# Kernel optimization log

Hardware: AMD Instinct MI355X
Metric: run time of the kernel (lower is better)

The kernel has to match this reference:

```python
import jax, jax.numpy as jnp
import numpy as np

B, C, N = 8, 128, 32768


def setup_inputs() -> dict:
    key = jax.random.key(0)
    ks = jax.random.split(key, 16)
    def g(k, shape, scale=0.05):
        return jax.random.normal(k, shape, dtype=jnp.float32) * scale
    return {
        "x": jax.random.normal(ks[0], (B, C, N), dtype=jnp.float32),
        "y": jax.random.normal(ks[1], (B, C, N), dtype=jnp.float32),
        "q_w": g(ks[2], (C, C)), "q_b": g(ks[3], (C,)),
        "k_w": g(ks[4], (C, C)), "k_b": g(ks[5], (C,)),
        "v1_w": g(ks[6], (C, C)), "v1_b": g(ks[7], (C,)),
        "v2_w": g(ks[8], (C, C)), "v2_b": g(ks[9], (C,)),
        "t1_w": g(ks[10], (2 * C, 2 * C)), "t1_b": g(ks[11], (2 * C,)),
        "t2_w": g(ks[12], (C, 2 * C)), "t2_b": g(ks[13], (C,)),
    }


def reference(x, y, q_w, q_b, k_w, k_b, v1_w, v1_b, v2_w, v2_b,
              t1_w, t1_b, t2_w, t2_b):
    # num_heads = 1, head_dim = C. Conv1d with kernel 1 == pointwise matmul.
    c = x.shape[1]
    pconv = lambda w, b, z: jnp.einsum('oc,bcn->bon', w, z) + b[None, :, None]
    x_q = pconv(q_w, q_b, y)    # [B,C,N]
    x_k = pconv(k_w, k_b, x)    # [B,C,N]
    x_v = pconv(v1_w, v1_b, x)  # [B,C,N]
    y_v = pconv(v2_w, v2_b, y)  # [B,C,N]
    x_con = jnp.concatenate([x_q, x_k], axis=1)                 # [B,2C,N]
    v_con = jnp.concatenate([y_v.transpose(0, 2, 1),
                             x_v.transpose(0, 2, 1)], axis=2)   # [B,N,2C]
    scale = jnp.sqrt(jnp.float32(2 * c))
    energy = jnp.einsum('bcn,bdn->bcd', x_con, x_con) / scale   # [B,2C,2C]
    e = jax.nn.relu(energy @ t1_w.T + t1_b)                     # [B,2C,2C]
    e = jax.nn.relu(e @ t2_w.T + t2_b)                          # [B,2C,C]
    attn = jax.nn.softmax(e, axis=-1)                           # [B,2C,C]
    x_r = jnp.einsum('bnd,bdc->bnc', v_con, attn)               # [B,N,C]
    return x_r.transpose(0, 2, 1)                               # [B,C,N]
```

## Files before the change

### kernel.cpp

```cpp
#include <hip/hip_runtime.h>

constexpr int CH   = 128;
constexpr int TWOC = 256;
constexpr int NPTS = 32768;
constexpr int NB   = 8;
constexpr int KC   = 2048;

constexpr int KC3    = 1024;
constexpr int KSTAGE = 128;
constexpr int NST    = KC3 / KSTAGE;
constexpr int NCHUNK = NPTS / KC3;

typedef _Float16 half8 __attribute__((ext_vector_type(8)));
typedef float floatx4 __attribute__((ext_vector_type(4)));

constexpr size_t OFF_G  = 0;
constexpr size_t OFF_S  = 524288;
constexpr size_t OFF_P  = 526336;
constexpr size_t OFF_H  = 528384;
constexpr size_t OFF_E  = 1052672;
constexpr size_t OFF_E1 = 1576960;
constexpr size_t OFF_E2 = 2101248;
constexpr size_t OFF_AT = 2363392;
constexpr size_t OFF_C0 = 2625536;
constexpr size_t OFF_MH = 2626560;
constexpr size_t OFF_ZH = 2757632;
constexpr size_t OFF_GP = OFF_ZH + 33554432;
constexpr size_t GP_LEN = (size_t)3 * NB * NCHUNK * 128 * 128;
constexpr size_t WS_NEED_NEW = (OFF_ZH + 33554432) * sizeof(float);
constexpr size_t WS_NEED_V3  = (OFF_GP + GP_LEN) * sizeof(float);


__global__ __launch_bounds__(256) void convert_kernel(
    const float* __restrict__ x, const float* __restrict__ y,
    _Float16* __restrict__ Zh, float* __restrict__ S)
{
  const int seg = blockIdx.x;
  const int r   = blockIdx.y;
  const int b   = blockIdx.z;
  const float* src = ((r < CH) ? (y + ((size_t)b*CH + r)*NPTS)
                               : (x + ((size_t)b*CH + (r-CH))*NPTS)) + (size_t)seg*4096;
  _Float16* dst = Zh + ((size_t)b*TWOC + r)*NPTS + (size_t)seg*4096;
  const int tid = threadIdx.x;

  float s = 0.f;
  #pragma unroll
  for (int it = 0; it < 4; it++) {
    const int idx = it*1024 + tid*4;
    const float4 v = *(const float4*)(src + idx);
    union { uint2 u; _Float16 h[4]; } p;
    p.h[0]=(_Float16)v.x; p.h[1]=(_Float16)v.y; p.h[2]=(_Float16)v.z; p.h[3]=(_Float16)v.w;
    *(uint2*)(dst + idx) = p.u;
    s += v.x + v.y + v.z + v.w;
  }

  for (int off = 32; off > 0; off >>= 1) s += __shfl_down(s, off);
  if ((tid & 63) == 0) atomicAdd(&S[b*TWOC + r], s);
}

__global__ __launch_bounds__(256) void gram_mfma3(
    const _Float16* __restrict__ Zh, float* __restrict__ G, float* __restrict__ GP)
{
  __shared__ __align__(16) _Float16 As[2][128 * KSTAGE];
  __shared__ __align__(16) _Float16 Bs[2][128 * KSTAGE];

  const int hw    = blockIdx.x;
  const int xcd   = hw & 7;
  const int local = hw >> 3;
  const int t     = local % 3;
  const int grp   = local / 3;
  const int gidx  = xcd * 32 + grp;
  const int kc    = gidx & 31;
  const int b     = gidx >> 5;

  const int i0 = (t == 0) ? 0 : CH;
  const int j0 = (t == 2) ? CH : 0;
  const _Float16* Ar = Zh + ((size_t)b*TWOC + i0)*NPTS + (size_t)kc*KC3;
  const _Float16* Br = Zh + ((size_t)b*TWOC + j0)*NPTS + (size_t)kc*KC3;

  const int tid   = threadIdx.x;
  const int lane  = tid & 63;
  const int wave  = tid >> 6;
  const int mbase = (wave & 1) * 64;
  const int nbase = (wave >> 1) * 64;
  const int m0    = lane & 15;
  const int quad  = lane >> 4;

#define STAGE(buf, k0)                                                        \
  {                                                                           \
    _Pragma("unroll")                                                         \
    for (int i = 0; i < 8; i++) {                                             \
      const int s = wave*512 + i*64 + lane;                                   \
      const int r = s >> 4;                                                   \
      const int g = s & 15;                                                   \
      const int gs = g ^ (r & 7);                                             \
      __builtin_amdgcn_global_load_lds(                                       \
        (const __attribute__((address_space(1))) void*)(Ar + (size_t)r*NPTS + (k0) + gs*8), \
        (__attribute__((address_space(3))) void*)&As[buf][(wave*512 + i*64)*8], \
        16, 0, 0);                                                            \
      __builtin_amdgcn_global_load_lds(                                       \
        (const __attribute__((address_space(1))) void*)(Br + (size_t)r*NPTS + (k0) + gs*8), \
        (__attribute__((address_space(3))) void*)&Bs[buf][(wave*512 + i*64)*8], \
        16, 0, 0);                                                            \
    }                                                                         \
  }

  floatx4 acc[4][4];
  #pragma unroll
  for (int i = 0; i < 4; i++)
    #pragma unroll
    for (int j = 0; j < 4; j++) acc[i][j] = (floatx4){0.f,0.f,0.f,0.f};

  STAGE(0, 0);

  int cur = 0;
  for (int st = 0; st < NST; ++st) {
    if (st + 1 < NST) {
      STAGE(cur ^ 1, (st + 1) * KSTAGE);
      asm volatile("s_waitcnt vmcnt(16)" ::: "memory");
    } else {
      asm volatile("s_waitcnt vmcnt(0)" ::: "memory");
    }
    __builtin_amdgcn_s_barrier();

    #pragma unroll
    for (int kk = 0; kk < 4; kk++) {
      half8 af[4], bf[4];
      #pragma unroll
      for (int i = 0; i < 4; i++) {
        const int ra = mbase + i*16 + m0;
        const int ga = (kk*4 + quad) ^ (ra & 7);
        af[i] = *(const half8*)&As[cur][ra*KSTAGE + ga*8];
        const int rb = nbase + i*16 + m0;
        const int gb = (kk*4 + quad) ^ (rb & 7);
        bf[i] = *(const half8*)&Bs[cur][rb*KSTAGE + gb*8];
      }
      #pragma unroll
      for (int i = 0; i < 4; i++)
        #pragma unroll
        for (int j = 0; j < 4; j++)
          acc[i][j] = __builtin_amdgcn_mfma_f32_16x16x32_f16(af[i], bf[j], acc[i][j], 0, 0, 0);
    }

    __builtin_amdgcn_s_barrier();
    cur ^= 1;
  }
#undef STAGE

  if (GP != nullptr) {
    float* gp = GP + (((size_t)(b*3 + t)*NCHUNK + kc) * (128*128));
    #pragma unroll
    for (int i = 0; i < 4; i++)
      #pragma unroll
      for (int j = 0; j < 4; j++)
        #pragma unroll
        for (int rg = 0; rg < 4; rg++) {
          const int row = mbase + i*16 + quad*4 + rg;
          const int col = nbase + j*16 + m0;
          gp[row*128 + col] = acc[i][j][rg];
        }
  } else {
    #pragma unroll
    for (int i = 0; i < 4; i++)
      #pragma unroll
      for (int j = 0; j < 4; j++)
        #pragma unroll
        for (int rg = 0; rg < 4; rg++) {
          const int row = i0 + mbase + i*16 + quad*4 + rg;
          const int col = j0 + nbase + j*16 + m0;
          atomicAdd(&G[((size_t)b*TWOC + row)*TWOC + col], acc[i][j][rg]);
        }
  }
}

__global__ __launch_bounds__(256) void greduce_kernel(
    const float* __restrict__ GP, float* __restrict__ G)
{
  const int t   = blockIdx.y;
  const int b   = blockIdx.z;
  const int idx = blockIdx.x * 256 + threadIdx.x;
  const float* gp = GP + ((size_t)(b*3 + t)*NCHUNK) * (128*128) + idx;
  float s = 0.f;
  #pragma unroll
  for (int k = 0; k < NCHUNK; k++) s += gp[(size_t)k * (128*128)];
  const int i0 = (t == 0) ? 0 : CH;
  const int j0 = (t == 2) ? CH : 0;
  const int row = idx >> 7, col = idx & 127;
  G[((size_t)b*TWOC + i0 + row)*TWOC + j0 + col] = s;
  if (t == 1)
    G[((size_t)b*TWOC + col)*TWOC + CH + row] = s;
}

__global__ __launch_bounds__(256) void att_row_kernel(
    const float* __restrict__ G, const float* __restrict__ S,
    const float* __restrict__ qw, const float* __restrict__ kw,
    const float* __restrict__ qb, const float* __restrict__ kb,
    const float* __restrict__ t1w, const float* __restrict__ t1b,
    const float* __restrict__ t2w, const float* __restrict__ t2b,
    float* __restrict__ ATT)
{
  const int i   = blockIdx.x;
  const int b   = blockIdx.y;
  const int tid = threadIdx.x;

  __shared__ float Hs[TWOC];
  __shared__ float Es[TWOC];
  __shared__ float E1s[TWOC];
  __shared__ float Ss[TWOC];
  __shared__ float red[8];

  Ss[tid] = S[b*TWOC + tid];

  const int jbase = (i < CH) ? 0 : CH;
  const float* wi  = (i < CH) ? (qw + (size_t)i*CH) : (kw + (size_t)(i-CH)*CH);
  const float bci  = (i < CH) ? qb[i] : kb[i-CH];

  float hacc = 0.f;
  const float* gcol = G + ((size_t)b*TWOC + jbase)*TWOC + tid;
  for (int j2 = 0; j2 < CH; j2++) hacc = fmaf(wi[j2], gcol[(size_t)j2*TWOC], hacc);
  Hs[tid] = hacc;
  __syncthreads();

  {
    const int j = tid;
    const float* wj = (j < CH) ? (qw + (size_t)j*CH) : (kw + (size_t)(j-CH)*CH);
    const float bcj = (j < CH) ? qb[j] : kb[j-CH];
    const float* hseg = Hs + ((j < CH) ? 0 : CH);
    const float* ssj  = Ss + ((j < CH) ? 0 : CH);
    const float* ssi  = Ss + ((i < CH) ? 0 : CH);
    const float4* w4  = (const float4*)wj;
    const float4* wi4 = (const float4*)wi;
    float eacc = 0.f, pj = 0.f, pi = 0.f;
    for (int k = 0; k < CH/4; k++) {
      const float4 wv  = w4[k];
      const float4 hv  = *(const float4*)&hseg[k*4];
      const float4 sv  = *(const float4*)&ssj[k*4];
      const float4 wiv = wi4[k];
      const float4 siv = *(const float4*)&ssi[k*4];
      eacc += hv.x*wv.x + hv.y*wv.y + hv.z*wv.z + hv.w*wv.w;
      pj   += sv.x*wv.x + sv.y*wv.y + sv.z*wv.z + sv.w*wv.w;
      pi   += siv.x*wiv.x + siv.y*wiv.y + siv.z*wiv.z + siv.w*wiv.w;
    }
    eacc += pi*bcj + bci*pj + (float)NPTS * bci * bcj;
    Es[j] = eacc * (1.0f/16.0f);
  }
  __syncthreads();

  {
    float a1 = t1b[tid];
    const float4* wr = (const float4*)(t1w + (size_t)tid*TWOC);
    for (int k = 0; k < TWOC/4; k++) {
      const float4 wv = wr[k];
      const float4 ev = *(const float4*)&Es[k*4];
      a1 += ev.x*wv.x + ev.y*wv.y + ev.z*wv.z + ev.w*wv.w;
    }
    E1s[tid] = fmaxf(a1, 0.f);
  }
  __syncthreads();

  float e2 = 0.f;
  if (tid < CH) {
    float a2 = t2b[tid];
    const float4* wr = (const float4*)(t2w + (size_t)tid*TWOC);
    for (int k = 0; k < TWOC/4; k++) {
      const float4 wv = wr[k];
      const float4 ev = *(const float4*)&E1s[k*4];
      a2 += ev.x*wv.x + ev.y*wv.y + ev.z*wv.z + ev.w*wv.w;
    }
    e2 = fmaxf(a2, 0.f);
  }

  const int lane = tid & 63, wv_ = tid >> 6;
  float m = (tid < CH) ? e2 : -1e30f;
  for (int off = 32; off > 0; off >>= 1) m = fmaxf(m, __shfl_xor(m, off));
  if (lane == 0) red[wv_] = m;
  __syncthreads();
  m = fmaxf(red[0], red[1]);

  float ex = (tid < CH) ? expf(e2 - m) : 0.f;
  float sum = ex;
  for (int off = 32; off > 0; off >>= 1) sum += __shfl_xor(sum, off);
  if (lane == 0) red[4 + wv_] = sum;
  __syncthreads();
  sum = red[4] + red[5];

  if (tid < CH)
    ATT[((size_t)b*TWOC + i)*CH + tid] = ex / sum;
}

__global__ __launch_bounds__(256) void out_mfma(
    const _Float16* __restrict__ Zh, const _Float16* __restrict__ Mh,
    const float* __restrict__ C0, float* __restrict__ out)
{
  const int n0 = blockIdx.x * 128;
  const int b  = blockIdx.y;

  __shared__ __align__(16) _Float16 As[128*64];
  __shared__ __align__(16) _Float16 Bs[128*72];

  const int tid   = threadIdx.x;
  const int lane  = tid & 63;
  const int wave  = tid >> 6;
  const int mbase = (wave & 1) * 64;
  const int nbase = (wave >> 1) * 64;
  const int m0    = lane & 15;
  const int quad  = lane >> 4;

  const int srow  = tid >> 1;
  const int gbase = (tid & 1) * 4;
  const int dl    = tid >> 4;
  const int ng    = tid & 15;

  floatx4 acc[4][4];
  #pragma unroll
  for (int i = 0; i < 4; i++)
    #pragma unroll
    for (int j = 0; j < 4; j++) acc[i][j] = (floatx4){0.f,0.f,0.f,0.f};

  for (int d0 = 0; d0 < TWOC; d0 += 64) {
    __syncthreads();
    #pragma unroll
    for (int q = 0; q < 4; q++) {
      const int g  = gbase + q;
      const int gp = g ^ (srow & 7);
      *(uint4*)&As[(size_t)(srow*8 + gp)*8] =
          *(const uint4*)(Mh + ((size_t)b*CH + srow)*TWOC + d0 + g*8);
    }
    #pragma unroll
    for (int ds = 0; ds < 4; ds++) {
      const int d    = dl + ds*16;
      const int gd   = d >> 3;
      const int dlow = d & 7;
      union { uint4 u; _Float16 h[8]; } v;
      v.u = *(const uint4*)(Zh + ((size_t)b*TWOC + d0 + d)*NPTS + n0 + ng*8);
      #pragma unroll
      for (int e = 0; e < 8; e++) {
        const int n  = ng*8 + e;
        const int pg = gd ^ (ng & 7);
        Bs[(size_t)n*72 + pg*8 + dlow] = v.h[e];
      }
    }
    __syncthreads();
    #pragma unroll
    for (int ks = 0; ks < 2; ks++) {
      half8 af[4], bf[4];
      #pragma unroll
      for (int i = 0; i < 4; i++) {
        const int ra = mbase + i*16 + m0;
        const int ga = (ks*4 + quad) ^ (ra & 7);
        af[i] = *(const half8*)&As[(size_t)(ra*8 + ga)*8];
        const int rn  = nbase + i*16 + m0;
        const int g   = ks*4 + quad;
        const int pgr = g ^ ((rn >> 3) & 7);
        bf[i] = *(const half8*)&Bs[(size_t)rn*72 + pgr*8];
      }
      #pragma unroll
      for (int i = 0; i < 4; i++)
        #pragma unroll
        for (int j = 0; j < 4; j++)
          acc[i][j] = __builtin_amdgcn_mfma_f32_16x16x32_f16(af[i], bf[j], acc[i][j], 0, 0, 0);
    }
  }

  #pragma unroll
  for (int i = 0; i < 4; i++) {
    #pragma unroll
    for (int rg = 0; rg < 4; rg++) {
      const int c  = mbase + i*16 + quad*4 + rg;
      const float cv = C0[b*CH + c];
      #pragma unroll
      for (int j = 0; j < 4; j++) {
        const int n = n0 + nbase + j*16 + m0;
        out[((size_t)b*CH + c)*NPTS + n] = acc[i][j][rg] + cv;
      }
    }
  }
}

__global__ void mout_f16_kernel(const float* __restrict__ ATT, const float* __restrict__ v1w,
                                const float* __restrict__ v2w, const float* __restrict__ v1b,
                                const float* __restrict__ v2b, _Float16* __restrict__ Mh,
                                float* __restrict__ C0)
{
  const int c = blockIdx.x, b = blockIdx.y, j = threadIdx.x;
  __shared__ float acol[TWOC];
  acol[j] = ATT[((size_t)b*TWOC + j)*CH + c];
  __syncthreads();
  float acc = 0.f;
  if (j < CH) {
    for (int d = 0; d < CH; d++) acc = fmaf(acol[d], v2w[(size_t)d*CH + j], acc);
  } else {
    const int jj = j - CH;
    for (int d = 0; d < CH; d++) acc = fmaf(acol[CH + d], v1w[(size_t)d*CH + jj], acc);
  }
  Mh[((size_t)b*CH + c)*TWOC + j] = (_Float16)acc;
  if (j == 0) {
    float s = 0.f;
    for (int d = 0; d < CH; d++) s += acol[d]*v2b[d] + acol[CH+d]*v1b[d];
    C0[b*CH + c] = s;
  }
}

__global__ void pmirror_kernel(const float* __restrict__ S, const float* __restrict__ qw,
                               const float* __restrict__ kw, float* __restrict__ P,
                               float* __restrict__ G)
{
  const int b = blockIdx.x;
  const int tid = threadIdx.x;
  float* Gb = G + (size_t)b * TWOC * TWOC;
  for (int idx = tid; idx < CH*CH; idx += 256) {
    const int i2 = idx >> 7, j2 = idx & 127;
    Gb[(size_t)i2*TWOC + CH + j2] = Gb[(size_t)(CH + j2)*TWOC + i2];
  }
}

__global__ __launch_bounds__(256) void gram_kernel(
    const float* __restrict__ x, const float* __restrict__ y,
    float* __restrict__ G, float* __restrict__ S)
{
  const int t  = blockIdx.x;
  const int kc = blockIdx.y;
  const int b  = blockIdx.z;
  const float* Ab = (t == 0) ? y : x;
  const float* Bb = (t == 2) ? x : y;
  const int growA = (t == 0) ? 0 : CH;
  const int gcolB = (t == 2) ? CH : 0;
  const float* Ap = Ab + (size_t)b * CH * NPTS + (size_t)kc * KC;
  const float* Bp = Bb + (size_t)b * CH * NPTS + (size_t)kc * KC;

  __shared__ __align__(16) float As[8][128];
  __shared__ __align__(16) float Bs[8][128];

  const int tid  = threadIdx.x;
  const int ti   = tid >> 4;
  const int tj   = tid & 15;
  const int lrow = tid >> 1;
  const int lk4  = (tid & 1) * 4;

  const float* arow = Ap + (size_t)lrow * NPTS + lk4;
  const float* brow = Bp + (size_t)lrow * NPTS + lk4;

  float acc[8][8];
  #pragma unroll
  for (int i = 0; i < 8; i++)
    #pragma unroll
    for (int j = 0; j < 8; j++) acc[i][j] = 0.f;
  float asum = 0.f;

  for (int k0 = 0; k0 < KC; k0 += 8) {
    const float4 av = *(const float4*)(arow + k0);
    const float4 bv = *(const float4*)(brow + k0);
    __syncthreads();
    As[lk4+0][lrow] = av.x; As[lk4+1][lrow] = av.y;
    As[lk4+2][lrow] = av.z; As[lk4+3][lrow] = av.w;
    Bs[lk4+0][lrow] = bv.x; Bs[lk4+1][lrow] = bv.y;
    Bs[lk4+2][lrow] = bv.z; Bs[lk4+3][lrow] = bv.w;
    asum += av.x + av.y + av.z + av.w;
    __syncthreads();
    #pragma unroll
    for (int kk = 0; kk < 8; kk++) {
      float a[8], bb[8];
      *(float4*)&a[0]  = *(const float4*)&As[kk][ti*8];
      *(float4*)&a[4]  = *(const float4*)&As[kk][ti*8+4];
      *(float4*)&bb[0] = *(const float4*)&Bs[kk][tj*8];
      *(float4*)&bb[4] = *(const float4*)&Bs[kk][tj*8+4];
      #pragma unroll
      for (int ii = 0; ii < 8; ii++)
        #pragma unroll
        for (int jj = 0; jj < 8; jj++)
          acc[ii][jj] = fmaf(a[ii], bb[jj], acc[ii][jj]);
    }
  }

  float* Gp = G + ((size_t)b * TWOC + growA) * TWOC + gcolB;
  #pragma unroll
  for (int ii = 0; ii < 8; ii++)
    #pragma unroll
    for (int jj = 0; jj < 8; jj++)
      atomicAdd(&Gp[(size_t)(ti*8+ii) * TWOC + (tj*8+jj)], acc[ii][jj]);

  if (t == 0)      atomicAdd(&S[b*TWOC + lrow],      asum);
  else if (t == 2) atomicAdd(&S[b*TWOC + CH + lrow], asum);
}

__global__ void mout_f32_kernel(const float* __restrict__ ATT, const float* __restrict__ v1w,
                                const float* __restrict__ v2w, const float* __restrict__ v1b,
                                const float* __restrict__ v2b, float* __restrict__ M,
                                float* __restrict__ C0)
{
  const int c = blockIdx.x, b = blockIdx.y, j = threadIdx.x;
  __shared__ float acol[TWOC];
  acol[j] = ATT[((size_t)b*TWOC + j)*CH + c];
  __syncthreads();
  float acc = 0.f;
  if (j < CH) {
    for (int d = 0; d < CH; d++) acc = fmaf(acol[d], v2w[(size_t)d*CH + j], acc);
  } else {
    const int jj = j - CH;
    for (int d = 0; d < CH; d++) acc = fmaf(acol[CH + d], v1w[(size_t)d*CH + jj], acc);
  }
  M[((size_t)b*CH + c)*TWOC + j] = acc;
  if (j == 0) {
    float s = 0.f;
    for (int d = 0; d < CH; d++) s += acol[d]*v2b[d] + acol[CH+d]*v1b[d];
    C0[b*CH + c] = s;
  }
}

__global__ __launch_bounds__(256) void out_kernel(
    const float* __restrict__ x, const float* __restrict__ y,
    const float* __restrict__ M, const float* __restrict__ C0,
    float* __restrict__ out)
{
  const int b  = blockIdx.y;
  const int n0 = blockIdx.x * 64;
  const int tid = threadIdx.x;
  const int tc = tid & 15;
  const int tn = tid >> 4;

  __shared__ __align__(16) float Ms[64][128];
  __shared__ __align__(16) float Zs[64][64];

  float acc[8][4];
  #pragma unroll
  for (int i = 0; i < 8; i++)
    #pragma unroll
    for (int j = 0; j < 4; j++) acc[i][j] = 0.f;

  const float* Mb = M + (size_t)b * CH * TWOC;

  for (int chunk = 0; chunk < 4; chunk++) {
    const int kbase = chunk * 64;
    const float* Zsrc = ((chunk < 2) ? y : x) + (size_t)b * CH * NPTS
                        + (size_t)((chunk & 1) * 64) * NPTS;
    __syncthreads();
    {
      const int c   = tid >> 1;
      const int kb2 = (tid & 1) * 32;
      const float* mr = Mb + (size_t)c * TWOC + kbase + kb2;
      #pragma unroll
      for (int q = 0; q < 8; q++) {
        const float4 v = *(const float4*)(mr + q*4);
        Ms[kb2 + q*4 + 0][c] = v.x;
        Ms[kb2 + q*4 + 1][c] = v.y;
        Ms[kb2 + q*4 + 2][c] = v.z;
        Ms[kb2 + q*4 + 3][c] = v.w;
      }
      const int kk  = tid >> 2;
      const int nb4 = (tid & 3) * 4;
      const float* zr = Zsrc + (size_t)kk * NPTS + n0 + nb4;
      #pragma unroll
      for (int q = 0; q < 4; q++)
        *(float4*)&Zs[kk][nb4 + q*16] = *(const float4*)(zr + q*16);
    }
    __syncthreads();
    #pragma unroll 8
    for (int kk = 0; kk < 64; kk++) {
      float a[8], zz[4];
      *(float4*)&a[0]  = *(const float4*)&Ms[kk][tc*8];
      *(float4*)&a[4]  = *(const float4*)&Ms[kk][tc*8+4];
      *(float4*)&zz[0] = *(const float4*)&Zs[kk][tn*4];
      #pragma unroll
      for (int ii = 0; ii < 8; ii++)
        #pragma unroll
        for (int jj = 0; jj < 4; jj++)
          acc[ii][jj] = fmaf(a[ii], zz[jj], acc[ii][jj]);
    }
  }

  #pragma unroll
  for (int ii = 0; ii < 8; ii++) {
    const int c = tc*8 + ii;
    const float cv = C0[b*CH + c];
    float4 o;
    o.x = acc[ii][0] + cv; o.y = acc[ii][1] + cv;
    o.z = acc[ii][2] + cv; o.w = acc[ii][3] + cv;
    *(float4*)&out[((size_t)b*CH + c)*NPTS + n0 + tn*4] = o;
  }
}

extern "C" void kernel_launch(void* const* d_in, const int* in_sizes, int n_in,
                              void* d_out, int out_size, void* d_ws, size_t ws_size,
                              hipStream_t stream)
{
  const float* x   = (const float*)d_in[0];
  const float* y   = (const float*)d_in[1];
  const float* qw  = (const float*)d_in[2];
  const float* qb  = (const float*)d_in[3];
  const float* kw  = (const float*)d_in[4];
  const float* kb  = (const float*)d_in[5];
  const float* v1w = (const float*)d_in[6];
  const float* v1b = (const float*)d_in[7];
  const float* v2w = (const float*)d_in[8];
  const float* v2b = (const float*)d_in[9];
  const float* t1w = (const float*)d_in[10];
  const float* t1b = (const float*)d_in[11];
  const float* t2w = (const float*)d_in[12];
  const float* t2b = (const float*)d_in[13];

  float* ws = (float*)d_ws;
  float* G  = ws + OFF_G;
  float* S  = ws + OFF_S;
  float* P  = ws + OFF_P;
  float* AT = ws + OFF_AT;
  float* C0 = ws + OFF_C0;
  float* outp = (float*)d_out;

  hipMemsetAsync(d_ws, 0, (OFF_S + 2048) * sizeof(float), stream);

  if (ws_size >= WS_NEED_NEW) {
    _Float16* Mh = (_Float16*)(ws + OFF_MH);
    _Float16* Zh = (_Float16*)(ws + OFF_ZH);
    const bool useGP = (ws_size >= WS_NEED_V3);
    float* GP = useGP ? (ws + OFF_GP) : nullptr;

    convert_kernel<<<dim3(NPTS/4096, TWOC, NB), 256, 0, stream>>>(x, y, Zh, S);
    gram_mfma3    <<<dim3(3 * NCHUNK * NB),     256, 0, stream>>>(Zh, G, GP);
    if (useGP)
      greduce_kernel<<<dim3(64, 3, NB),         256, 0, stream>>>(GP, G);
    else
      pmirror_kernel<<<dim3(NB),                256, 0, stream>>>(S, qw, kw, P, G);
    att_row_kernel<<<dim3(TWOC, NB),            256, 0, stream>>>(G, S, qw, kw, qb, kb,
                                                                  t1w, t1b, t2w, t2b, AT);
    mout_f16_kernel<<<dim3(CH, NB),             256, 0, stream>>>(AT, v1w, v2w, v1b, v2b, Mh, C0);
    out_mfma      <<<dim3(NPTS/128, NB),        256, 0, stream>>>(Zh, Mh, C0, outp);
  } else {
    float* Mo = ws + OFF_MH;
    gram_kernel   <<<dim3(3, NPTS/KC, NB), 256, 0, stream>>>(x, y, G, S);
    pmirror_kernel<<<dim3(NB),             256, 0, stream>>>(S, qw, kw, P, G);
    att_row_kernel<<<dim3(TWOC, NB),       256, 0, stream>>>(G, S, qw, kw, qb, kb,
                                                             t1w, t1b, t2w, t2b, AT);
    mout_f32_kernel<<<dim3(CH, NB),        256, 0, stream>>>(AT, v1w, v2w, v1b, v2b, Mo, C0);
    out_kernel    <<<dim3(NPTS/64, NB),    256, 0, stream>>>(x, y, Mo, C0, outp);
  }
}
```

Baseline: 615.5 us.

## Batch attention rows per block with transposed weights and precomputed P

```diff
diff --git a/kernel.cpp b/kernel.cpp
--- a/kernel.cpp
+++ b/kernel.cpp
@@ -18,9 +18,6 @@
 constexpr size_t OFF_S  = 524288;
 constexpr size_t OFF_P  = 526336;
 constexpr size_t OFF_H  = 528384;
-constexpr size_t OFF_E  = 1052672;
-constexpr size_t OFF_E1 = 1576960;
-constexpr size_t OFF_E2 = 2101248;
 constexpr size_t OFF_AT = 2363392;
 constexpr size_t OFF_C0 = 2625536;
 constexpr size_t OFF_MH = 2626560;
@@ -29,6 +26,10 @@
 constexpr size_t GP_LEN = (size_t)3 * NB * NCHUNK * 128 * 128;
 constexpr size_t WS_NEED_NEW = (OFF_ZH + 33554432) * sizeof(float);
 constexpr size_t WS_NEED_V3  = (OFF_GP + GP_LEN) * sizeof(float);
+
+constexpr size_t OFF_WQKT = OFF_H;
+constexpr size_t OFF_T1T  = OFF_H + 32768;
+constexpr size_t OFF_T2T  = OFF_H + 32768 + 65536;
 
 
 __global__ __launch_bounds__(256) void convert_kernel(
@@ -191,101 +192,188 @@
     G[((size_t)b*TWOC + col)*TWOC + CH + row] = s;
 }
 
-__global__ __launch_bounds__(256) void att_row_kernel(
-    const float* __restrict__ G, const float* __restrict__ S,
+__global__ void wtrans_kernel(const float* __restrict__ qw, const float* __restrict__ kw,
+                              const float* __restrict__ t1w, const float* __restrict__ t2w,
+                              float* __restrict__ wqkT, float* __restrict__ t1wT,
+                              float* __restrict__ t2wT)
+{
+  const int r = blockIdx.x;
+  const int j = threadIdx.x;
+  if (r < 128) {
+    wqkT[(size_t)r*TWOC + j] = (j < CH) ? qw[(size_t)j*CH + r] : kw[(size_t)(j-CH)*CH + r];
+  } else if (r < 384) {
+    const int k = r - 128;
+    t1wT[(size_t)k*TWOC + j] = t1w[(size_t)j*TWOC + k];
+  } else {
+    const int k = r - 384;
+    if (j < CH) t2wT[(size_t)k*CH + j] = t2w[(size_t)j*TWOC + k];
+  }
+}
+
+__global__ void p_kernel(const float* __restrict__ S, const float* __restrict__ qw,
+                         const float* __restrict__ kw, float* __restrict__ P)
+{
+  const int b = blockIdx.x;
+  const int i = threadIdx.x;
+  const float* w = (i < CH) ? (qw + (size_t)i*CH) : (kw + (size_t)(i-CH)*CH);
+  const float* s = S + b*TWOC + ((i < CH) ? 0 : CH);
+  float acc = 0.f;
+  for (int k = 0; k < CH; k++) acc = fmaf(w[k], s[k], acc);
+  P[b*TWOC + i] = acc;
+}
+
+__global__ __launch_bounds__(256) void he_att_kernel(
+    const float* __restrict__ G, const float* __restrict__ P_,
     const float* __restrict__ qw, const float* __restrict__ kw,
     const float* __restrict__ qb, const float* __restrict__ kb,
-    const float* __restrict__ t1w, const float* __restrict__ t1b,
-    const float* __restrict__ t2w, const float* __restrict__ t2b,
-    float* __restrict__ ATT)
-{
-  const int i   = blockIdx.x;
-  const int b   = blockIdx.y;
+    const float* __restrict__ wqkT, const float* __restrict__ t1wT,
+    const float* __restrict__ t2wT, const float* __restrict__ t1b,
+    const float* __restrict__ t2b, float* __restrict__ ATT)
+{
+  const int it = blockIdx.x;
+  const int b  = blockIdx.y;
+  const int i0 = it * 8;
+  const bool hi = (i0 >= CH);
+  const int jb = hi ? CH : 0;
+
+  __shared__ float Ws[8][CH];
+  __shared__ float As[8][TWOC];
+  __shared__ float Es[8][TWOC];
+  __shared__ float E1s[8][TWOC];
+  __shared__ float E2s[8][CH];
+  __shared__ float Ps[TWOC];
+  __shared__ float Bc[TWOC];
+  __shared__ float bci[8];
+
   const int tid = threadIdx.x;
-
-  __shared__ float Hs[TWOC];
-  __shared__ float Es[TWOC];
-  __shared__ float E1s[TWOC];
-  __shared__ float Ss[TWOC];
-  __shared__ float red[8];
-
-  Ss[tid] = S[b*TWOC + tid];
-
-  const int jbase = (i < CH) ? 0 : CH;
-  const float* wi  = (i < CH) ? (qw + (size_t)i*CH) : (kw + (size_t)(i-CH)*CH);
-  const float bci  = (i < CH) ? qb[i] : kb[i-CH];
-
-  float hacc = 0.f;
-  const float* gcol = G + ((size_t)b*TWOC + jbase)*TWOC + tid;
-  for (int j2 = 0; j2 < CH; j2++) hacc = fmaf(wi[j2], gcol[(size_t)j2*TWOC], hacc);
-  Hs[tid] = hacc;
+  const int tx  = tid & 63;
+  const int ty  = tid >> 6;
+  const int r0  = ty * 2;
+  const int r1  = r0 + 1;
+
+  {
+    const int rr = tid >> 5;
+    const int cc = (tid & 31) * 4;
+    const float* wr = hi ? (kw + (size_t)(i0 - CH + rr)*CH)
+                         : (qw + (size_t)(i0 + rr)*CH);
+    *(float4*)&Ws[rr][cc] = *(const float4*)&wr[cc];
+  }
+  Ps[tid] = P_[b*TWOC + tid];
+  Bc[tid] = (tid < CH) ? qb[tid] : kb[tid - CH];
+  if (tid < 8) bci[tid] = hi ? kb[i0 - CH + tid] : qb[i0 + tid];
   __syncthreads();
 
   {
-    const int j = tid;
-    const float* wj = (j < CH) ? (qw + (size_t)j*CH) : (kw + (size_t)(j-CH)*CH);
-    const float bcj = (j < CH) ? qb[j] : kb[j-CH];
-    const float* hseg = Hs + ((j < CH) ? 0 : CH);
-    const float* ssj  = Ss + ((j < CH) ? 0 : CH);
-    const float* ssi  = Ss + ((i < CH) ? 0 : CH);
-    const float4* w4  = (const float4*)wj;
-    const float4* wi4 = (const float4*)wi;
-    float eacc = 0.f, pj = 0.f, pi = 0.f;
-    for (int k = 0; k < CH/4; k++) {
-      const float4 wv  = w4[k];
-      const float4 hv  = *(const float4*)&hseg[k*4];
-      const float4 sv  = *(const float4*)&ssj[k*4];
-      const float4 wiv = wi4[k];
-      const float4 siv = *(const float4*)&ssi[k*4];
-      eacc += hv.x*wv.x + hv.y*wv.y + hv.z*wv.z + hv.w*wv.w;
-      pj   += sv.x*wv.x + sv.y*wv.y + sv.z*wv.z + sv.w*wv.w;
-      pi   += siv.x*wiv.x + siv.y*wiv.y + siv.z*wiv.z + siv.w*wiv.w;
-    }
-    eacc += pi*bcj + bci*pj + (float)NPTS * bci * bcj;
-    Es[j] = eacc * (1.0f/16.0f);
+    const float* gb = G + ((size_t)b*TWOC + jb)*TWOC + tx*4;
+    floatx4 a0 = {0,0,0,0}, a1 = {0,0,0,0};
+    #pragma unroll 4
+    for (int j = 0; j < CH; j++) {
+      const float4 g4 = *(const float4*)(gb + (size_t)j*TWOC);
+      const float w0 = Ws[r0][j], w1 = Ws[r1][j];
+      a0[0] = fmaf(w0, g4.x, a0[0]); a0[1] = fmaf(w0, g4.y, a0[1]);
+      a0[2] = fmaf(w0, g4.z, a0[2]); a0[3] = fmaf(w0, g4.w, a0[3]);
+      a1[0] = fmaf(w1, g4.x, a1[0]); a1[1] = fmaf(w1, g4.y, a1[1]);
+      a1[2] = fmaf(w1, g4.z, a1[2]); a1[3] = fmaf(w1, g4.w, a1[3]);
+    }
+    *(floatx4*)&As[r0][tx*4] = a0;
+    *(floatx4*)&As[r1][tx*4] = a1;
   }
   __syncthreads();
 
   {
-    float a1 = t1b[tid];
-    const float4* wr = (const float4*)(t1w + (size_t)tid*TWOC);
-    for (int k = 0; k < TWOC/4; k++) {
-      const float4 wv = wr[k];
-      const float4 ev = *(const float4*)&Es[k*4];
-      a1 += ev.x*wv.x + ev.y*wv.y + ev.z*wv.z + ev.w*wv.w;
-    }
-    E1s[tid] = fmaxf(a1, 0.f);
+    const int jc = tx * 4;
+    const int sj = (jc < CH) ? 0 : CH;
+    const float* wt = wqkT + jc;
+    floatx4 e0 = {0,0,0,0}, e1 = {0,0,0,0};
+    #pragma unroll 4
+    for (int k = 0; k < CH; k++) {
+      const float4 w4 = *(const float4*)(wt + (size_t)k*TWOC);
+      const float a0 = As[r0][sj + k], a1 = As[r1][sj + k];
+      e0[0] = fmaf(a0, w4.x, e0[0]); e0[1] = fmaf(a0, w4.y, e0[1]);
+      e0[2] = fmaf(a0, w4.z, e0[2]); e0[3] = fmaf(a0, w4.w, e0[3]);
+      e1[0] = fmaf(a1, w4.x, e1[0]); e1[1] = fmaf(a1, w4.y, e1[1]);
+      e1[2] = fmaf(a1, w4.z, e1[2]); e1[3] = fmaf(a1, w4.w, e1[3]);
+    }
+    const float4 pj = *(const float4*)&Ps[jc];
+    const float4 bj = *(const float4*)&Bc[jc];
+    const float pi0 = Ps[i0 + r0], pi1 = Ps[i0 + r1];
+    const float bi0 = bci[r0],     bi1 = bci[r1];
+    const float NN = (float)NPTS;
+    floatx4 o0, o1;
+    o0[0] = (e0[0] + bi0*pj.x + bj.x*pi0 + NN*bi0*bj.x) * (1.0f/16.0f);
+    o0[1] = (e0[1] + bi0*pj.y + bj.y*pi0 + NN*bi0*bj.y) * (1.0f/16.0f);
+    o0[2] = (e0[2] + bi0*pj.z + bj.z*pi0 + NN*bi0*bj.z) * (1.0f/16.0f);
+    o0[3] = (e0[3] + bi0*pj.w + bj.w*pi0 + NN*bi0*bj.w) * (1.0f/16.0f);
+    o1[0] = (e1[0] + bi1*pj.x + bj.x*pi1 + NN*bi1*bj.x) * (1.0f/16.0f);
+    o1[1] = (e1[1] + bi1*pj.y + bj.y*pi1 + NN*bi1*bj.y) * (1.0f/16.0f);
+    o1[2] = (e1[2] + bi1*pj.z + bj.z*pi1 + NN*bi1*bj.z) * (1.0f/16.0f);
+    o1[3] = (e1[3] + bi1*pj.w + bj.w*pi1 + NN*bi1*bj.w) * (1.0f/16.0f);
+    *(floatx4*)&Es[r0][jc] = o0;
+    *(floatx4*)&Es[r1][jc] = o1;
   }
   __syncthreads();
 
-  float e2 = 0.f;
-  if (tid < CH) {
-    float a2 = t2b[tid];
-    const float4* wr = (const float4*)(t2w + (size_t)tid*TWOC);
-    for (int k = 0; k < TWOC/4; k++) {
-      const float4 wv = wr[k];
-      const float4 ev = *(const float4*)&E1s[k*4];
-      a2 += ev.x*wv.x + ev.y*wv.y + ev.z*wv.z + ev.w*wv.w;
-    }
-    e2 = fmaxf(a2, 0.f);
-  }
-
-  const int lane = tid & 63, wv_ = tid >> 6;
-  float m = (tid < CH) ? e2 : -1e30f;
-  for (int off = 32; off > 0; off >>= 1) m = fmaxf(m, __shfl_xor(m, off));
-  if (lane == 0) red[wv_] = m;
+  {
+    const int jc = tx * 4;
+    const float* wt = t1wT + jc;
+    floatx4 a0 = {0,0,0,0}, a1 = {0,0,0,0};
+    #pragma unroll 4
+    for (int k = 0; k < TWOC; k++) {
+      const float4 w4 = *(const float4*)(wt + (size_t)k*TWOC);
+      const float e0 = Es[r0][k], e1 = Es[r1][k];
+      a0[0] = fmaf(e0, w4.x, a0[0]); a0[1] = fmaf(e0, w4.y, a0[1]);
+      a0[2] = fmaf(e0, w4.z, a0[2]); a0[3] = fmaf(e0, w4.w, a0[3]);
+      a1[0] = fmaf(e1, w4.x, a1[0]); a1[1] = fmaf(e1, w4.y, a1[1]);
+      a1[2] = fmaf(e1, w4.z, a1[2]); a1[3] = fmaf(e1, w4.w, a1[3]);
+    }
+    const float4 b1v = *(const float4*)&t1b[jc];
+    floatx4 o0, o1;
+    o0[0] = fmaxf(a0[0] + b1v.x, 0.f); o0[1] = fmaxf(a0[1] + b1v.y, 0.f);
+    o0[2] = fmaxf(a0[2] + b1v.z, 0.f); o0[3] = fmaxf(a0[3] + b1v.w, 0.f);
+    o1[0] = fmaxf(a1[0] + b1v.x, 0.f); o1[1] = fmaxf(a1[1] + b1v.y, 0.f);
+    o1[2] = fmaxf(a1[2] + b1v.z, 0.f); o1[3] = fmaxf(a1[3] + b1v.w, 0.f);
+    *(floatx4*)&E1s[r0][jc] = o0;
+    *(floatx4*)&E1s[r1][jc] = o1;
+  }
   __syncthreads();
-  m = fmaxf(red[0], red[1]);
-
-  float ex = (tid < CH) ? expf(e2 - m) : 0.f;
-  float sum = ex;
-  for (int off = 32; off > 0; off >>= 1) sum += __shfl_xor(sum, off);
-  if (lane == 0) red[4 + wv_] = sum;
+
+  {
+    const int jc2 = (tid & 31) * 4;
+    const int r   = tid >> 5;
+    const float* wt = t2wT + jc2;
+    floatx4 a = {0,0,0,0};
+    #pragma unroll 4
+    for (int k = 0; k < TWOC; k++) {
+      const float4 w4 = *(const float4*)(wt + (size_t)k*CH);
+      const float e = E1s[r][k];
+      a[0] = fmaf(e, w4.x, a[0]); a[1] = fmaf(e, w4.y, a[1]);
+      a[2] = fmaf(e, w4.z, a[2]); a[3] = fmaf(e, w4.w, a[3]);
+    }
+    const float4 b2v = *(const float4*)&t2b[jc2];
+    floatx4 o;
+    o[0] = fmaxf(a[0] + b2v.x, 0.f); o[1] = fmaxf(a[1] + b2v.y, 0.f);
+    o[2] = fmaxf(a[2] + b2v.z, 0.f); o[3] = fmaxf(a[3] + b2v.w, 0.f);
+    *(floatx4*)&E2s[r][jc2] = o;
+  }
   __syncthreads();
-  sum = red[4] + red[5];
-
-  if (tid < CH)
-    ATT[((size_t)b*TWOC + i)*CH + tid] = ex / sum;
+
+  {
+    const int l = tx;
+    #pragma unroll
+    for (int rr = 0; rr < 2; rr++) {
+      const int r = ty*2 + rr;
+      const float v0 = E2s[r][l], v1 = E2s[r][l + 64];
+      float m = fmaxf(v0, v1);
+      for (int off = 32; off > 0; off >>= 1) m = fmaxf(m, __shfl_xor(m, off));
+      const float ex0 = expf(v0 - m), ex1 = expf(v1 - m);
+      float s = ex0 + ex1;
+      for (int off = 32; off > 0; off >>= 1) s += __shfl_xor(s, off);
+      const float inv = 1.f / s;
+      float* o = ATT + ((size_t)b*TWOC + i0 + r)*CH;
+      o[l] = ex0 * inv;
+      o[l + 64] = ex1 * inv;
+    }
+  }
 }
 
 __global__ __launch_bounds__(256) void out_mfma(
@@ -401,9 +489,7 @@
   }
 }
 
-__global__ void pmirror_kernel(const float* __restrict__ S, const float* __restrict__ qw,
-                               const float* __restrict__ kw, float* __restrict__ P,
-                               float* __restrict__ G)
+__global__ void pmirror_kernel(float* __restrict__ G)
 {
   const int b = blockIdx.x;
   const int tid = threadIdx.x;
@@ -599,11 +685,14 @@
   const float* t2b = (const float*)d_in[13];
 
   float* ws = (float*)d_ws;
-  float* G  = ws + OFF_G;
-  float* S  = ws + OFF_S;
-  float* P  = ws + OFF_P;
-  float* AT = ws + OFF_AT;
-  float* C0 = ws + OFF_C0;
+  float* G    = ws + OFF_G;
+  float* S    = ws + OFF_S;
+  float* P    = ws + OFF_P;
+  float* wqkT = ws + OFF_WQKT;
+  float* t1wT = ws + OFF_T1T;
+  float* t2wT = ws + OFF_T2T;
+  float* AT   = ws + OFF_AT;
+  float* C0   = ws + OFF_C0;
   float* outp = (float*)d_out;
 
   hipMemsetAsync(d_ws, 0, (OFF_S + 2048) * sizeof(float), stream);
@@ -614,22 +703,30 @@
     const bool useGP = (ws_size >= WS_NEED_V3);
     float* GP = useGP ? (ws + OFF_GP) : nullptr;
 
+    wtrans_kernel <<<dim3(640),                 256, 0, stream>>>(qw, kw, t1w, t2w,
+                                                                  wqkT, t1wT, t2wT);
     convert_kernel<<<dim3(NPTS/4096, TWOC, NB), 256, 0, stream>>>(x, y, Zh, S);
     gram_mfma3    <<<dim3(3 * NCHUNK * NB),     256, 0, stream>>>(Zh, G, GP);
     if (useGP)
       greduce_kernel<<<dim3(64, 3, NB),         256, 0, stream>>>(GP, G);
     else
-      pmirror_kernel<<<dim3(NB),                256, 0, stream>>>(S, qw, kw, P, G);
-    att_row_kernel<<<dim3(TWOC, NB),            256, 0, stream>>>(G, S, qw, kw, qb, kb,
-                                                                  t1w, t1b, t2w, t2b, AT);
+      pmirror_kernel<<<dim3(NB),                256, 0, stream>>>(G);
+    p_kernel      <<<dim3(NB),                  256, 0, stream>>>(S, qw, kw, P);
+    he_att_kernel <<<dim3(32, NB),              256, 0, stream>>>(G, P, qw, kw, qb, kb,
+                                                                  wqkT, t1wT, t2wT,
+                                                                  t1b, t2b, AT);
     mout_f16_kernel<<<dim3(CH, NB),             256, 0, stream>>>(AT, v1w, v2w, v1b, v2b, Mh, C0);
     out_mfma      <<<dim3(NPTS/128, NB),        256, 0, stream>>>(Zh, Mh, C0, outp);
   } else {
     float* Mo = ws + OFF_MH;
+    wtrans_kernel <<<dim3(640),            256, 0, stream>>>(qw, kw, t1w, t2w,
+                                                             wqkT, t1wT, t2wT);
     gram_kernel   <<<dim3(3, NPTS/KC, NB), 256, 0, stream>>>(x, y, G, S);
-    pmirror_kernel<<<dim3(NB),             256, 0, stream>>>(S, qw, kw, P, G);
-    att_row_kernel<<<dim3(TWOC, NB),       256, 0, stream>>>(G, S, qw, kw, qb, kb,
-                                                             t1w, t1b, t2w, t2b, AT);
+    pmirror_kernel<<<dim3(NB),             256, 0, stream>>>(G);
+    p_kernel      <<<dim3(NB),             256, 0, stream>>>(S, qw, kw, P);
+    he_att_kernel <<<dim3(32, NB),         256, 0, stream>>>(G, P, qw, kw, qb, kb,
+                                                             wqkT, t1wT, t2wT,
+                                                             t1b, t2b, AT);
     mout_f32_kernel<<<dim3(CH, NB),        256, 0, stream>>>(AT, v1w, v2w, v1b, v2b, Mo, C0);
     out_kernel    <<<dim3(NPTS/64, NB),    256, 0, stream>>>(x, y, Mo, C0, outp);
   }
```

Measured after the change: 582.0 us. -5.4%, faster.
